# Performance work log

Hardware: AMD Instinct MI355X
Metric: run time of the kernel (lower is better)

Reference implementation:

```python
import jax, jax.numpy as jnp
import numpy as np
from jax import lax

NF, CF, LAT = 128, 3, 512          # n_filter, sobel c_factor (id+gx+gy), lat_size
NL, NC = 3, 4                      # n_layers (img 64 -> 3), n_calls
B, IMG, CH = 16, 64, 3
FIN, FH, FOUT = NF * CF, NF, 2 * NF  # dyna/res block in, hidden, out (gated -> 2*NF)
SPLIT = [NF, NF, NF, 1]
NOUT = sum(SPLIT)                  # 385
CS = NF + NF * 16 + NF * 16 + 16 * 16  # 4480 multi-cut state size
SEG = [FIN * FH, FH, FH * FH, FH, FH * FOUT, FOUT, FIN * FOUT, FOUT]
OFF = np.concatenate([[0], np.cumsum(SEG)]).astype(int)
K = int(OFF[-1])                   # hypernet output size (197376)

SOBEL_X = jnp.array([[-1., 0., 1.], [-2., 0., 2.], [-1., 0., 1.]], jnp.float32) / 8.0
SOBEL_Y = SOBEL_X.T
_g = np.exp(-0.5 * (np.arange(3) - 1.0) ** 2); _g /= _g.sum()
GAUSS = jnp.asarray(np.outer(_g, _g), jnp.float32)  # 3x3 gaussian, sigma=1


def dwconv(x, k2d):
    # depthwise conv, same 3x3 kernel for every channel, padding 1
    C = x.shape[1]
    k = jnp.broadcast_to(k2d.astype(x.dtype), (C, 1, 3, 3))
    return lax.conv_general_dilated(x, k, (1, 1), ((1, 1), (1, 1)),
                                    dimension_numbers=('NCHW', 'OIHW', 'NCHW'),
                                    feature_group_count=C)


def instnorm(x, eps=1e-5):
    m = x.mean((2, 3), keepdims=True)
    v = x.var((2, 3), keepdims=True)
    return (x - m) * lax.rsqrt(v + eps)


def conv1x1(x, w, b):  # w: [O, C]
    return jnp.einsum('bchw,oc->bohw', x, w) + b[None, :, None, None]


def lrb(x, w1, b1, w2, b2, wsc, bsc):  # LinearResidualBlock
    return x @ wsc.T + bsc + jax.nn.relu(x @ w1.T + b1) @ w2.T + b2


def _w(k, shape, fan_in):
    return jax.random.normal(k, shape, jnp.float32) / np.sqrt(fan_in)


def setup_inputs():
    ks = jax.random.split(jax.random.key(0), 24)
    z = lambda *s: jnp.zeros(s, jnp.float32)
    d = {}
    d['x'] = jax.random.normal(ks[0], (B, CH, IMG, IMG), jnp.float32)
    d['inj_lat'] = jax.random.normal(ks[1], (B, LAT), jnp.float32)
    d['leak_factor'] = jnp.float32(0.1)
    d['in_w'] = _w(ks[2], (NF, CH), CH); d['in_b'] = z(NF)
    d['fc_w1'] = _w(ks[3], (FH, FIN), FIN); d['fc_b1'] = z(FH)
    d['fc_w2'] = _w(ks[4], (FOUT, FH), FH); d['fc_b2'] = z(FOUT)
    d['fc_wsc'] = _w(ks[5], (FOUT, FIN), FIN); d['fc_bsc'] = z(FOUT)
    d['hyp_w'] = _w(ks[6], (K, LAT), LAT) * 0.1; d['hyp_b'] = z(K)
    d['lat_w'] = _w(ks[7], (NL * NC, LAT, LAT), LAT); d['lat_b'] = z(NL * NC, LAT)
    d['seed'] = _w(ks[8], (1, NF, 16, 16), NF)
    d['out_w'] = _w(ks[9], (NOUT, NF), NF); d['out_b'] = z(NOUT)
    d['l1_w1'] = _w(ks[10], (2 * LAT, CS), CS); d['l1_b1'] = z(2 * LAT)
    d['l1_w2'] = _w(ks[11], (LAT, 2 * LAT), 2 * LAT); d['l1_b2'] = z(LAT)
    d['l1_wsc'] = _w(ks[12], (LAT, CS), CS); d['l1_bsc'] = z(LAT)
    d['l2_w1'] = _w(ks[13], (LAT, LAT), LAT); d['l2_b1'] = z(LAT)
    d['l2_w2'] = _w(ks[14], (LAT, LAT), LAT); d['l2_b2'] = z(LAT)
    d['l2_wsc'] = _w(ks[15], (LAT, LAT), LAT); d['l2_bsc'] = z(LAT)
    d['fin_w'] = _w(ks[16], (LAT, LAT), LAT); d['fin_b'] = z(LAT)
    return d


def _forward(x, inj_lat, leak_factor, in_w, in_b, fc_w1, fc_b1, fc_w2, fc_b2,
             fc_wsc, fc_bsc, hyp_w, hyp_b, lat_w, lat_b, seed, out_w, out_b,
             l1_w1, l1_b1, l1_w2, l1_b2, l1_wsc, l1_bsc,
             l2_w1, l2_b1, l2_w2, l2_b2, l2_wsc, l2_bsc, fin_w, fin_b):
    out = conv1x1(x, in_w, in_b)
    leak = jnp.clip(leak_factor, 0.001, 1000.0)
    for c in range(NL * NC):
        # perception: identity + x/y sobel (c_factor=3), then instance norm
        p = jnp.concatenate([out, dwconv(out, SOBEL_X), dwconv(out, SOBEL_Y)], 1)
        p = instnorm(p)
        # static ResidualBlock (shared params)
        f = conv1x1(p, fc_wsc, fc_bsc) + conv1x1(jax.nn.relu(conv1x1(p, fc_w1, fc_b1)), fc_w2, fc_b2)
        # per-call latent expansion + hypernetwork -> per-sample 1x1 conv weights
        latc = inj_lat @ lat_w[c].T + lat_b[c]
        hk = latc @ hyp_w.T + hyp_b  # [B, K]
        w_in = hk[:, OFF[0]:OFF[1]].reshape(-1, FH, FIN); b_in = hk[:, OFF[1]:OFF[2]]
        w_md = hk[:, OFF[2]:OFF[3]].reshape(-1, FH, FH);  b_md = hk[:, OFF[3]:OFF[4]]
        w_ot = hk[:, OFF[4]:OFF[5]].reshape(-1, FOUT, FH); b_ot = hk[:, OFF[5]:OFF[6]]
        w_sc = hk[:, OFF[6]:OFF[7]].reshape(-1, FOUT, FIN); b_sc = hk[:, OFF[7]:OFF[8]]
        h = jax.nn.relu(jnp.einsum('bchw,boc->bohw', p, w_in) + b_in[:, :, None, None])
        h = jax.nn.relu(jnp.einsum('bchw,boc->bohw', h, w_md) + b_md[:, :, None, None])
        d = (jnp.einsum('bchw,boc->bohw', p, w_sc) + b_sc[:, :, None, None]
             + jnp.einsum('bchw,boc->bohw', h, w_ot) + b_ot[:, :, None, None])
        out_new = f + d  # [B, 2*NF, H, W]
        a, g = out_new[:, :NF], out_new[:, NF:]
        out = out + leak * (a * jax.nn.sigmoid(g))
        if c < NL * NC - 1 and c % NC == NC - 1:
            s = dwconv(out, GAUSS)
            # bilinear 0.5 downscale (align_corners=False) == 2x2 average
            Bn, C, H, W = s.shape
            out = s.reshape(Bn, C, H // 2, 2, W // 2, 2).mean((3, 5))
    out = out + seed  # broadcast seed [1, NF, 16, 16]
    o = conv1x1(out, out_w, out_b)  # [B, 385, 16, 16]
    f_, fh_, fw_, hw_ = o[:, :NF], o[:, NF:2 * NF], o[:, 2 * NF:3 * NF], o[:, 3 * NF:]
    bs = o.shape[0]
    cs = jnp.concatenate([f_.mean((2, 3)), fh_.mean(3).reshape(bs, -1),
                          fw_.mean(2).reshape(bs, -1), hw_.reshape(bs, -1)], 1)  # [B, 4480]
    hcs = lrb(cs, l1_w1, l1_b1, l1_w2, l1_b2, l1_wsc, l1_bsc)
    hcs = lrb(hcs, l2_w1, l2_b1, l2_w2, l2_b2, l2_wsc, l2_bsc)
    return hcs @ fin_w.T + fin_b  # [B, LAT]


def reference(x, inj_lat, leak_factor, in_w, in_b, fc_w1, fc_b1, fc_w2, fc_b2,
              fc_wsc, fc_bsc, hyp_w, hyp_b, lat_w, lat_b, seed, out_w, out_b,
              l1_w1, l1_b1, l1_w2, l1_b2, l1_wsc, l1_bsc,
              l2_w1, l2_b1, l2_w2, l2_b2, l2_wsc, l2_bsc, fin_w, fin_b):
    return _forward(x, inj_lat, leak_factor, in_w, in_b, fc_w1, fc_b1, fc_w2, fc_b2,
                    fc_wsc, fc_bsc, hyp_w, hyp_b, lat_w, lat_b, seed, out_w, out_b,
                    l1_w1, l1_b1, l1_w2, l1_b2, l1_wsc, l1_bsc,
                    l2_w1, l2_b1, l2_w2, l2_b2, l2_wsc, l2_bsc, fin_w, fin_b)
```

## Files before the change

kernel.cpp:

```cpp
#include <hip/hip_runtime.h>
#include <hip/hip_bf16.h>

typedef __hip_bfloat16 bf16;
typedef __attribute__((ext_vector_type(8))) short bf8_t;
typedef __attribute__((ext_vector_type(4))) float f4_t;

#define KHK 197376
#define OFF_WIN 0
#define OFF_BIN 49152
#define OFF_WMD 49280
#define OFF_BMD 65664
#define OFF_WOT 65792
#define OFF_BOT 98560
#define OFF_WSC 98816
#define OFF_BSC 197120

__device__ __forceinline__ float ldf(const float* p, size_t i){ return p[i]; }
__device__ __forceinline__ float ldf(const bf16* p, size_t i){ return __bfloat162float(p[i]); }
__device__ __forceinline__ void stf(float* p, size_t i, float v){ p[i] = v; }
__device__ __forceinline__ void stf(bf16* p, size_t i, float v){ p[i] = __float2bfloat16(v); }
__device__ __forceinline__ float b2f(short u){ return __uint_as_float(((unsigned)(unsigned short)u) << 16); }

typedef const __attribute__((address_space(1))) unsigned int* gas_t;
typedef __attribute__((address_space(3))) unsigned int* las_t;
__device__ __forceinline__ void gld_lds16(const void* g, void* l){
  __builtin_amdgcn_global_load_lds((gas_t)g, (las_t)l, 16, 0, 0);
}

struct Seg { const bf16* p; int klen; int ld; };

__global__ __launch_bounds__(256) void k_cvt_bf16(const float* __restrict__ in,
    bf16* __restrict__ out, size_t n){
  size_t stride = (size_t)gridDim.x * 256;
  for (size_t i = blockIdx.x*256ULL + threadIdx.x; i*8 < n; i += stride){
    float4 a = *reinterpret_cast<const float4*>(in + i*8);
    float4 c = *reinterpret_cast<const float4*>(in + i*8 + 4);
    union { bf8_t v; bf16 e[8]; } o;
    o.e[0]=__float2bfloat16(a.x); o.e[1]=__float2bfloat16(a.y);
    o.e[2]=__float2bfloat16(a.z); o.e[3]=__float2bfloat16(a.w);
    o.e[4]=__float2bfloat16(c.x); o.e[5]=__float2bfloat16(c.y);
    o.e[6]=__float2bfloat16(c.z); o.e[7]=__float2bfloat16(c.w);
    *reinterpret_cast<bf8_t*>(out + i*8) = o.v;
  }
}

__global__ __launch_bounds__(256) void k_in_conv(const float* __restrict__ x,
    const float* __restrict__ w, const float* __restrict__ b, float* __restrict__ out){
  int idx = blockIdx.x*256 + threadIdx.x;
  int c = idx & 127;
  int s = (idx >> 7) & 4095;
  int bi = idx >> 19;
  const float* xb = x + (size_t)bi*3*4096;
  out[idx] = b[c] + w[c*3]*xb[s] + w[c*3+1]*xb[4096+s] + w[c*3+2]*xb[8192+s];
}

__global__ __launch_bounds__(256) void k_sobel4(const float* __restrict__ src,
    bf16* __restrict__ p, int H, int S){
  int idx = blockIdx.x*256 + threadIdx.x;
  int c4 = (idx & 31) * 4;
  int s = (idx >> 5) % S;
  int b = idx / (S*32);
  int y = s / H, x = s - y*H;
  const float* sb = src + (size_t)b*S*128 + c4;
  float4 n[3][3];
  #pragma unroll
  for (int dy=0; dy<3; dy++)
    #pragma unroll
    for (int dx=0; dx<3; dx++){
      int yy = y + dy - 1, xx = x + dx - 1;
      if (yy>=0 && yy<H && xx>=0 && xx<H)
        n[dy][dx] = *reinterpret_cast<const float4*>(sb + (size_t)(yy*H+xx)*128);
      else
        n[dy][dx] = (float4){0.f,0.f,0.f,0.f};
    }
  float v0[4], sx[4], sy[4];
  #pragma unroll
  for (int q = 0; q < 4; q++){
    float e00=((const float*)&n[0][0])[q], e01=((const float*)&n[0][1])[q], e02=((const float*)&n[0][2])[q];
    float e10=((const float*)&n[1][0])[q], e11=((const float*)&n[1][1])[q], e12=((const float*)&n[1][2])[q];
    float e20=((const float*)&n[2][0])[q], e21=((const float*)&n[2][1])[q], e22=((const float*)&n[2][2])[q];
    v0[q] = e11;
    sx[q] = (-e00 + e02 - 2.f*e10 + 2.f*e12 - e20 + e22) * 0.125f;
    sy[q] = (-e00 - 2.f*e01 - e02 + e20 + 2.f*e21 + e22) * 0.125f;
  }
  bf16* pb = p + ((size_t)b*S + s)*384;
  union { unsigned long long u; bf16 e[4]; } o0, o1, o2;
  #pragma unroll
  for (int q = 0; q < 4; q++){
    o0.e[q] = __float2bfloat16(v0[q]);
    o1.e[q] = __float2bfloat16(sx[q]);
    o2.e[q] = __float2bfloat16(sy[q]);
  }
  *reinterpret_cast<unsigned long long*>(pb + c4)       = o0.u;
  *reinterpret_cast<unsigned long long*>(pb + 128 + c4) = o1.u;
  *reinterpret_cast<unsigned long long*>(pb + 256 + c4) = o2.u;
}

__global__ __launch_bounds__(256) void k_stats(const bf16* __restrict__ P_,
    float* __restrict__ SUMS, int S){
  __shared__ float sS[384], sQ[384];
  int b = blockIdx.y;
  int chunk = S >> 4;
  int s0 = blockIdx.x * chunk;
  int t = threadIdx.x;
  for (int i = t; i < 384; i += 256){ sS[i] = 0.f; sQ[i] = 0.f; }
  __syncthreads();
  if (t < 240){
    int oct = t % 48, ls = t / 48;
    int c8 = oct*8;
    float as[8] = {}, qs[8] = {};
    for (int s = s0 + ls; s < s0 + chunk; s += 5){
      bf8_t v = *reinterpret_cast<const bf8_t*>(P_ + ((size_t)b*S + s)*384 + c8);
      #pragma unroll
      for (int i=0;i<8;i++){ float f = b2f(v[i]); as[i]+=f; qs[i]+=f*f; }
    }
    #pragma unroll
    for (int i=0;i<8;i++){ atomicAdd(&sS[c8+i], as[i]); atomicAdd(&sQ[c8+i], qs[i]); }
  }
  __syncthreads();
  for (int i = t; i < 384; i += 256){
    atomicAdd(&SUMS[((size_t)b*384+i)*2],   sS[i]);
    atomicAdd(&SUMS[((size_t)b*384+i)*2+1], sQ[i]);
  }
}

__global__ __launch_bounds__(256) void k_hyper_all(const float* __restrict__ hw,
    const float* __restrict__ hb, const bf16* __restrict__ latb,
    bf16* __restrict__ hk_all){
  __shared__ float Sw[128][17];
  int h0 = blockIdx.x * 128;
  int tid = threadIdx.x, wid = tid >> 6, lane = tid & 63;
  int lr = lane & 15, lg = lane >> 4;
  f4_t acc[2][12];
  #pragma unroll
  for (int f=0; f<2; f++)
    #pragma unroll
    for (int j=0; j<12; j++) acc[f][j] = (f4_t){0.f,0.f,0.f,0.f};
  for (int k0 = 0; k0 < 512; k0 += 32){
    bf8_t af[2];
    #pragma unroll
    for (int f = 0; f < 2; f++){
      int h = h0 + wid*32 + f*16 + lr;
      const float* src = hw + (size_t)h*512 + k0 + lg*8;
      float4 x0 = *reinterpret_cast<const float4*>(src);
      float4 x1 = *reinterpret_cast<const float4*>(src + 4);
      union { bf8_t v; bf16 e[8]; } o;
      o.e[0]=__float2bfloat16(x0.x); o.e[1]=__float2bfloat16(x0.y);
      o.e[2]=__float2bfloat16(x0.z); o.e[3]=__float2bfloat16(x0.w);
      o.e[4]=__float2bfloat16(x1.x); o.e[5]=__float2bfloat16(x1.y);
      o.e[6]=__float2bfloat16(x1.z); o.e[7]=__float2bfloat16(x1.w);
      af[f] = o.v;
    }
    #pragma unroll
    for (int j = 0; j < 12; j++){
      bf8_t bv = *reinterpret_cast<const bf8_t*>(latb + (size_t)(j*16 + lr)*512 + k0 + lg*8);
      acc[0][j] = __builtin_amdgcn_mfma_f32_16x16x32_bf16(af[0], bv, acc[0][j], 0, 0, 0);
      acc[1][j] = __builtin_amdgcn_mfma_f32_16x16x32_bf16(af[1], bv, acc[1][j], 0, 0, 0);
    }
  }
  for (int j = 0; j < 12; j++){
    __syncthreads();
    #pragma unroll
    for (int f = 0; f < 2; f++)
      #pragma unroll
      for (int r = 0; r < 4; r++)
        Sw[wid*32 + f*16 + lg*4 + r][lr] = acc[f][j][r];
    __syncthreads();
    int bb = tid >> 4, h8 = (tid & 15) * 8;
    union { bf8_t v; bf16 e[8]; } o;
    #pragma unroll
    for (int i = 0; i < 8; i++)
      o.e[i] = __float2bfloat16(hb[h0 + h8 + i] + Sw[h8 + i][bb]);
    *reinterpret_cast<bf8_t*>(hk_all + ((size_t)j*16 + bb)*KHK + h0 + h8) = o.v;
  }
}

__global__ __launch_bounds__(256) void k_latall(const float* __restrict__ inj,
    const float* __restrict__ lat_w, const float* __restrict__ lat_b,
    bf16* __restrict__ LATB){
  int gwave = (int)((blockIdx.x*256 + threadIdx.x) >> 6);
  int lane = threadIdx.x & 63;
  int c = gwave >> 9, o = gwave & 511;
  const float* wr = lat_w + (size_t)c*262144 + (size_t)o*512;
  float acc[16] = {};
  for (int k = lane; k < 512; k += 64){
    float wv = wr[k];
    #pragma unroll
    for (int b = 0; b < 16; b++) acc[b] += wv * inj[b*512 + k];
  }
  #pragma unroll
  for (int b = 0; b < 16; b++)
    for (int off = 32; off > 0; off >>= 1) acc[b] += __shfl_down(acc[b], off);
  if (lane == 0){
    float bv = lat_b[c*512 + o];
    #pragma unroll
    for (int b = 0; b < 16; b++)
      LATB[(size_t)c*8192 + b*512 + o] = __float2bfloat16(acc[b] + bv);
  }
}

__global__ __launch_bounds__(256) void k_xform(
    const float* __restrict__ fc_w1, const float* __restrict__ fc_b1,
    const float* __restrict__ fc_w2, const float* __restrict__ fc_b2,
    const float* __restrict__ fc_wsc, const float* __restrict__ fc_bsc,
    const bf16* __restrict__ HK_, const float* __restrict__ SUMS, float Sf,
    bf16* __restrict__ Wstack, float* __restrict__ bstack,
    bf16* __restrict__ Wbig, float* __restrict__ bbig,
    bf16* __restrict__ Wmd, float* __restrict__ bmd){
  int gw = (blockIdx.x*256 + threadIdx.x) >> 6;
  int lane = threadIdx.x & 63;
  float invSf = 1.f / Sf;
  if (gw < 4096){
    int b = gw >> 8, o = gw & 255;
    const float* su = SUMS + (size_t)b*768;
    const bf16* hkb = HK_ + (size_t)b*KHK;
    float b0 = (o < 128) ? fc_b1[o] : ldf(hkb, OFF_BIN + (o-128));
    float accv = 0.f;
    bf16* dst = Wstack + ((size_t)b*256 + o)*384;
    for (int k = lane; k < 384; k += 64){
      float m = su[k*2] * invSf;
      float iv = rsqrtf(fmaxf(su[k*2+1]*invSf - m*m, 0.f) + 1e-5f);
      float wv = (o < 128) ? fc_w1[(size_t)o*384 + k]
                           : ldf(hkb, OFF_WIN + (size_t)(o-128)*384 + k);
      float w = wv * iv;
      accv += w * m;
      dst[k] = __float2bfloat16(w);
    }
    for (int off=32; off>0; off>>=1) accv += __shfl_down(accv, off);
    if (lane==0) bstack[b*256+o] = b0 - accv;
  } else if (gw < 8192){
    int r = gw - 4096; int b = r >> 8, o = r & 255;
    const float* su = SUMS + (size_t)b*768;
    const bf16* hkb = HK_ + (size_t)b*KHK;
    int cc = o & 127;
    int nr = ((cc >> 4) << 5) + ((o >> 7) << 4) + (cc & 15);
    bf16* dst = Wbig + ((size_t)b*256 + nr)*640;
    float accv = 0.f;
    for (int k = lane; k < 384; k += 64){
      float m = su[k*2] * invSf;
      float iv = rsqrtf(fmaxf(su[k*2+1]*invSf - m*m, 0.f) + 1e-5f);
      float w = (fc_wsc[(size_t)o*384 + k] + ldf(hkb, OFF_WSC + (size_t)o*384 + k)) * iv;
      accv += w * m;
      dst[k] = __float2bfloat16(w);
    }
    for (int k = lane; k < 128; k += 64){
      dst[384+k] = __float2bfloat16(fc_w2[(size_t)o*128 + k]);
      dst[512+k] = hkb[OFF_WOT + (size_t)o*128 + k];
    }
    for (int off=32; off>0; off>>=1) accv += __shfl_down(accv, off);
    if (lane==0) bbig[b*256+nr] = fc_bsc[o] + ldf(hkb, OFF_BSC+o) + fc_b2[o]
                                  + ldf(hkb, OFF_BOT+o) - accv;
  } else {
    int r = gw - 8192; int b = r >> 7, o = r & 127;
    const bf16* hkb = HK_ + (size_t)b*KHK;
    bf16* dst = Wmd + ((size_t)b*128 + o)*128;
    for (int k = lane; k < 128; k += 64)
      dst[k] = hkb[OFF_WMD + (size_t)o*128 + k];
    if (lane==0) bmd[b*128+o] = ldf(hkb, OFF_BMD + o);
  }
}

template<int RELU, int NSEG, int FUSE, class TOUT>
__global__ __launch_bounds__(256) void k_mfgemm(
    Seg s1, Seg s2, Seg s3,
    const bf16* __restrict__ W, long long wbstride, int Ktot,
    const float* __restrict__ bias, int bbstride,
    TOUT* __restrict__ OUTp, int ldc, int Mout, int S,
    const float* __restrict__ leakp){
  __shared__ short As[128][32];
  __shared__ short Bs[128][32];
  int b  = blockIdx.z;
  int s0 = blockIdx.x * 128;
  int n0 = blockIdx.y * 128;
  int tid = threadIdx.x;
  int wid = tid >> 6, lane = tid & 63;
  int wrow = (wid >> 1) * 64;
  int wcol = (wid & 1) * 64;
  int lr = lane & 15, lg = lane >> 4;
  int r0 = wid*32 + (lane >> 2);
  int c8 = (lane & 3) * 8;
  const bf16* Wb = W + (size_t)b * wbstride;
  f4_t acc[4][4] = {{}};
  int kbase = 0;
  #pragma unroll
  for (int si = 0; si < NSEG; si++){
    Seg sg = (si == 0) ? s1 : (si == 1) ? s2 : s3;
    const bf16* INb = sg.p + (size_t)b * S * sg.ld;
    const bf16* gA0 = INb + (size_t)(s0 + r0) * sg.ld + c8;
    const bf16* gA1 = INb + (size_t)(s0 + r0 + 16) * sg.ld + c8;
    const bf16* gB0 = Wb + (size_t)(n0 + r0) * Ktot + kbase + c8;
    const bf16* gB1 = Wb + (size_t)(n0 + r0 + 16) * Ktot + kbase + c8;
    for (int k0 = 0; k0 < sg.klen; k0 += 32){
      gld_lds16(gA0 + k0, &As[wid*32][0]);
      gld_lds16(gA1 + k0, &As[wid*32 + 16][0]);
      gld_lds16(gB0 + k0, &Bs[wid*32][0]);
      gld_lds16(gB1 + k0, &Bs[wid*32 + 16][0]);
      __syncthreads();
      bf8_t af[4], bfv[4];
      #pragma unroll
      for (int i = 0; i < 4; i++) af[i]  = *(const bf8_t*)(&As[wrow + i*16 + lr][lg*8]);
      #pragma unroll
      for (int j = 0; j < 4; j++) bfv[j] = *(const bf8_t*)(&Bs[wcol + j*16 + lr][lg*8]);
      #pragma unroll
      for (int i = 0; i < 4; i++)
        #pragma unroll
        for (int j = 0; j < 4; j++)
          acc[i][j] = __builtin_amdgcn_mfma_f32_16x16x32_bf16(af[i], bfv[j], acc[i][j], 0, 0, 0);
      __syncthreads();
    }
    kbase += sg.klen;
  }
  if (FUSE){
    float leak = fminf(fmaxf(leakp[0], 0.001f), 1000.f);
    float* OUTf = (float*)OUTp;
    #pragma unroll
    for (int jp = 0; jp < 2; jp++){
      int na = n0 + wcol + jp*32 + lr;
      float bva = bias[(size_t)b * bbstride + na];
      float bvg = bias[(size_t)b * bbstride + na + 16];
      int chan = ((n0 + wcol) >> 1) + jp*16 + lr;
      #pragma unroll
      for (int i = 0; i < 4; i++){
        int sr = s0 + wrow + i*16 + lg*4;
        #pragma unroll
        for (int r = 0; r < 4; r++){
          float av = acc[i][jp*2][r]   + bva;
          float gv = acc[i][jp*2+1][r] + bvg;
          size_t oidx = ((size_t)b * S + sr + r) * 128 + chan;
          OUTf[oidx] += leak * av * (1.f / (1.f + expf(-gv)));
        }
      }
    }
  } else {
    #pragma unroll
    for (int j = 0; j < 4; j++){
      int n = n0 + wcol + j*16 + lr;
      if (n >= Mout) continue;
      float bv = bias[(size_t)b * bbstride + n];
      #pragma unroll
      for (int i = 0; i < 4; i++){
        int sr = s0 + wrow + i*16 + lg*4;
        size_t base = ((size_t)b * S + sr) * ldc + n;
        #pragma unroll
        for (int r = 0; r < 4; r++){
          float v = acc[i][j][r] + bv;
          if (RELU) v = fmaxf(v, 0.f);
          stf(OUTp, base + (size_t)r * ldc, v);
        }
      }
    }
  }
}

__global__ __launch_bounds__(256) void k_blurpool(const float* __restrict__ src,
    float* __restrict__ dst, int H2, int S2){
  const float g[3] = {0.27406862f, 0.45186276f, 0.27406862f};
  int idx = blockIdx.x*256 + threadIdx.x;
  int c = idx & 127;
  int s2 = (idx >> 7) % S2;
  int b = idx / (S2*128);
  int y2 = s2 / H2, x2 = s2 - y2*H2;
  int H = H2*2;
  const float* sb = src + (size_t)b*(H*H)*128 + c;
  float acc = 0.f;
  #pragma unroll
  for (int dy2 = 0; dy2 < 2; dy2++)
    #pragma unroll
    for (int dx2 = 0; dx2 < 2; dx2++){
      int y = 2*y2 + dy2, x = 2*x2 + dx2;
      float bl = 0.f;
      #pragma unroll
      for (int i = 0; i < 3; i++)
        #pragma unroll
        for (int j = 0; j < 3; j++){
          int yy = y + i - 1, xx = x + j - 1;
          float v = (yy>=0 && yy<H && xx>=0 && xx<H) ? sb[(size_t)(yy*H+xx)*128] : 0.f;
          bl += v * g[i] * g[j];
        }
      acc += bl;
    }
  dst[idx] = acc * 0.25f;
}

__global__ __launch_bounds__(256) void k_seed(float* __restrict__ out,
    const float* __restrict__ seed){
  int idx = blockIdx.x*256 + threadIdx.x;
  int c = idx & 127;
  int s = (idx >> 7) & 255;
  out[idx] += seed[c*256 + s];
}

__global__ __launch_bounds__(256) void k_build_cs(const float* __restrict__ O,
    float* __restrict__ cs){
  int b = blockIdx.x;
  const float* Ob = O + (size_t)b*256*385;
  for (int id = threadIdx.x; id < 4480; id += 256){
    float v;
    if (id < 128){
      float s = 0; for (int t = 0; t < 256; t++) s += Ob[(size_t)t*385 + id];
      v = s * (1.f/256.f);
    } else if (id < 2176){
      int r = id - 128; int c = r >> 4, h = r & 15;
      float s = 0; for (int w = 0; w < 16; w++) s += Ob[(size_t)(h*16+w)*385 + 128 + c];
      v = s * (1.f/16.f);
    } else if (id < 4224){
      int r = id - 2176; int c = r >> 4, w = r & 15;
      float s = 0; for (int h = 0; h < 16; h++) s += Ob[(size_t)(h*16+w)*385 + 256 + c];
      v = s * (1.f/16.f);
    } else {
      v = Ob[(size_t)(id - 4224)*385 + 384];
    }
    cs[b*4480 + id] = v;
  }
}

template<int RELU, int ACCUM, class TOUT>
__global__ __launch_bounds__(256) void k_rowgemm(const float* __restrict__ IN,
    const float* __restrict__ W,
    const float* __restrict__ bias,
    TOUT* __restrict__ OUT, int M, int K){
  int wave = (int)((blockIdx.x*256 + threadIdx.x) >> 6);
  int lane = threadIdx.x & 63;
  if (wave >= M) return;
  const float* wr = W + (size_t)wave*K;
  float acc[16] = {};
  for (int k = lane; k < K; k += 64){
    float wv = wr[k];
    #pragma unroll
    for (int b = 0; b < 16; b++) acc[b] += wv * IN[b*K + k];
  }
  #pragma unroll
  for (int b = 0; b < 16; b++)
    for (int off = 32; off > 0; off >>= 1) acc[b] += __shfl_down(acc[b], off);
  if (lane == 0){
    float bv = bias[wave];
    #pragma unroll
    for (int b = 0; b < 16; b++){
      float v = acc[b] + bv;
      if (RELU) v = fmaxf(v, 0.f);
      size_t oi = (size_t)b*M + wave;
      if (ACCUM) v += ldf(OUT, oi);
      stf(OUT, oi, v);
    }
  }
}

template<int RELU1>
__global__ __launch_bounds__(256) void k_rowgemm2(const float* __restrict__ IN,
    const float* __restrict__ W1, const float* __restrict__ b1, float* __restrict__ O1, int M1,
    const float* __restrict__ W2, const float* __restrict__ b2, float* __restrict__ O2, int M2,
    int K){
  int wave = (int)((blockIdx.x*256 + threadIdx.x) >> 6);
  int lane = threadIdx.x & 63;
  if (wave >= M1 + M2) return;
  int second = (wave >= M1);
  int o = second ? (wave - M1) : wave;
  const float* wr = (second ? W2 : W1) + (size_t)o*K;
  float acc[16] = {};
  for (int k = lane; k < K; k += 64){
    float wv = wr[k];
    #pragma unroll
    for (int b = 0; b < 16; b++) acc[b] += wv * IN[b*K + k];
  }
  #pragma unroll
  for (int b = 0; b < 16; b++)
    for (int off = 32; off > 0; off >>= 1) acc[b] += __shfl_down(acc[b], off);
  if (lane == 0){
    float bv = second ? b2[o] : b1[o];
    float* OUT = second ? O2 : O1;
    int M = second ? M2 : M1;
    #pragma unroll
    for (int b = 0; b < 16; b++){
      float v = acc[b] + bv;
      if (RELU1 && !second) v = fmaxf(v, 0.f);
      OUT[(size_t)b*M + o] = v;
    }
  }
}

extern "C" void kernel_launch(void* const* d_in, const int* in_sizes, int n_in,
                              void* d_out, int out_size, void* d_ws, size_t ws_size,
                              hipStream_t stream){
  (void)in_sizes; (void)n_in; (void)out_size; (void)ws_size;
  const float* x      = (const float*)d_in[0];
  const float* inj    = (const float*)d_in[1];
  const float* leakp  = (const float*)d_in[2];
  const float* in_w   = (const float*)d_in[3];
  const float* in_b   = (const float*)d_in[4];
  const float* fc_w1  = (const float*)d_in[5];
  const float* fc_b1  = (const float*)d_in[6];
  const float* fc_w2  = (const float*)d_in[7];
  const float* fc_b2  = (const float*)d_in[8];
  const float* fc_wsc = (const float*)d_in[9];
  const float* fc_bsc = (const float*)d_in[10];
  const float* hyp_w  = (const float*)d_in[11];
  const float* hyp_b  = (const float*)d_in[12];
  const float* lat_w  = (const float*)d_in[13];
  const float* lat_b  = (const float*)d_in[14];
  const float* seed   = (const float*)d_in[15];
  const float* out_w  = (const float*)d_in[16];
  const float* out_b  = (const float*)d_in[17];
  const float* l1_w1  = (const float*)d_in[18];
  const float* l1_b1  = (const float*)d_in[19];
  const float* l1_w2  = (const float*)d_in[20];
  const float* l1_b2  = (const float*)d_in[21];
  const float* l1_wsc = (const float*)d_in[22];
  const float* l1_bsc = (const float*)d_in[23];
  const float* l2_w1  = (const float*)d_in[24];
  const float* l2_b1  = (const float*)d_in[25];
  const float* l2_w2  = (const float*)d_in[26];
  const float* l2_b2  = (const float*)d_in[27];
  const float* l2_wsc = (const float*)d_in[28];
  const float* l2_bsc = (const float*)d_in[29];
  const float* fin_w  = (const float*)d_in[30];
  const float* fin_b  = (const float*)d_in[31];

  char* ws = (char*)d_ws;
  float* OUT    = (float*)(ws);
  bf16*  P      = (bf16*)(ws + 33554432UL);
  bf16*  HG     = (bf16*)(ws + 83886080UL);
  bf16*  G2     = (bf16*)(ws + 117440512UL);
  bf16*  HKALL  = (bf16*)(ws + 134217728UL);
  bf16*  WSTK   = (bf16*)(ws + 285802496UL);
  bf16*  WBIG   = (bf16*)(ws + 288948224UL);
  bf16*  WMD    = (bf16*)(ws + 294191104UL);
  float* BSTK   = (float*)(ws + 294715392UL);
  float* BBIG   = (float*)(ws + 294731776UL);
  float* BMD    = (float*)(ws + 294748160UL);
  bf16*  LATB   = (bf16*)(ws + 294805504UL);
  bf16*  OUTB   = (bf16*)(ws + 295002112UL);
  float* OHEAD  = (float*)(ws + 296050688UL);
  bf16*  OWB    = (bf16*)(ws + 302358528UL);
  float* CS     = (float*)(ws + 302457088UL);
  float* T1     = (float*)(ws + 302743808UL);
  float* HCS    = (float*)(ws + 302809344UL);
  float* HCS2   = (float*)(ws + 302842112UL);
  float* SUMS12 = (float*)(ws + 302874880UL);
  float* OUT2   = (float*)(ws + 310378496UL);

  k_cvt_bf16<<<32, 256, 0, stream>>>(out_w, OWB, 49280ULL);
  k_in_conv<<<32768, 256, 0, stream>>>(x, in_w, in_b, OUT);

  k_latall<<<1536, 256, 0, stream>>>(inj, lat_w, lat_b, LATB);
  k_hyper_all<<<1542, 256, 0, stream>>>(hyp_w, hyp_b, LATB, HKALL);
  hipMemsetAsync(SUMS12, 0, 12*16*384*2*sizeof(float), stream);

  float* cur = OUT;
  float* alt = OUT2;
  int H = 64;
  for (int c = 0; c < 12; c++){
    int S = H*H;
    float* SUMS = SUMS12 + (size_t)c*16*768;
    k_sobel4<<<(16*S*32)/256, 256, 0, stream>>>(cur, P, H, S);
    k_stats<<<dim3(16,16), 256, 0, stream>>>(P, SUMS, S);
    k_xform<<<2560, 256, 0, stream>>>(fc_w1, fc_b1, fc_w2, fc_b2, fc_wsc, fc_bsc,
                                      HKALL + (size_t)c*16*KHK, SUMS, (float)S,
                                      WSTK, BSTK, WBIG, BBIG, WMD, BMD);
    Seg segP  = {P, 384, 384};
    Seg segH1 = {HG, 128, 256};
    Seg segHm = {HG + 128, 128, 256};
    Seg segG2 = {G2, 128, 128};
    k_mfgemm<1,1,0,bf16><<<dim3(S/128, 2, 16), 256, 0, stream>>>(
        segP, segP, segP, WSTK, 98304LL, 384, BSTK, 256, HG, 256, 256, S, nullptr);
    k_mfgemm<1,1,0,bf16><<<dim3(S/128, 1, 16), 256, 0, stream>>>(
        segHm, segHm, segHm, WMD, 16384LL, 128, BMD, 128, G2, 128, 128, S, nullptr);
    k_mfgemm<0,3,1,float><<<dim3(S/128, 2, 16), 256, 0, stream>>>(
        segP, segH1, segG2, WBIG, 163840LL, 640, BBIG, 256, cur, 128, 256, S, leakp);
    if (c == 3 || c == 7){
      int H2 = H/2, S2 = S/4;
      k_blurpool<<<(16*S2*128)/256, 256, 0, stream>>>(cur, alt, H2, S2);
      float* t = cur; cur = alt; alt = t;
      H = H2;
    }
  }

  k_seed<<<2048, 256, 0, stream>>>(cur, seed);
  k_cvt_bf16<<<256, 256, 0, stream>>>(cur, OUTB, 524288ULL);
  Seg segO = {OUTB, 128, 128};
  k_mfgemm<0,1,0,float><<<dim3(2, 4, 16), 256, 0, stream>>>(
      segO, segO, segO, OWB, 0LL, 128, out_b, 0, OHEAD, 385, 385, 256, nullptr);
  k_build_cs<<<16, 256, 0, stream>>>(OHEAD, CS);

  k_rowgemm2<1><<<384, 256, 0, stream>>>(CS, l1_w1, l1_b1, T1, 1024,
                                         l1_wsc, l1_bsc, HCS, 512, 4480);
  k_rowgemm<0,1,float><<<128, 256, 0, stream>>>(T1, l1_w2, l1_b2, HCS, 512, 1024);
  k_rowgemm2<1><<<256, 256, 0, stream>>>(HCS, l2_w1, l2_b1, T1, 512,
                                         l2_wsc, l2_bsc, HCS2, 512, 512);
  k_rowgemm<0,1,float><<<128, 256, 0, stream>>>(T1, l2_w2, l2_b2, HCS2, 512, 512);
  k_rowgemm<0,0,float><<<128, 256, 0, stream>>>(HCS2, fin_w, fin_b, (float*)d_out, 512, 512);
}
```

Before: 1.553 ms.

## Fuse middle GEMM into final gated GEMM via LDS-resident G2 tile

The hidden-layer GEMM (HG[:,128:] x Wmd) is now computed inside the final gated GEMM kernel, and its ReLU output G2 stays in shared memory instead of going through global memory. This removes one kernel launch per call and the global write and read of G2. The cost is that the middle GEMM is recomputed by both n-blocks (blockIdx.y = 0 and 1), and the extra ~34KB of LDS may lower occupancy. The seed add and bf16 conversion are also merged into one kernel.

```diff
diff --git a/kernel.cpp b/kernel.cpp
--- a/kernel.cpp
+++ b/kernel.cpp
@@ -260,13 +260,12 @@
   }
 }
 
-template<int RELU, int NSEG, int FUSE, class TOUT>
+template<int RELU, int NSEG, class TOUT>
 __global__ __launch_bounds__(256) void k_mfgemm(
     Seg s1, Seg s2, Seg s3,
     const bf16* __restrict__ W, long long wbstride, int Ktot,
     const float* __restrict__ bias, int bbstride,
-    TOUT* __restrict__ OUTp, int ldc, int Mout, int S,
-    const float* __restrict__ leakp){
+    TOUT* __restrict__ OUTp, int ldc, int Mout, int S){
   __shared__ short As[128][32];
   __shared__ short Bs[128][32];
   int b  = blockIdx.z;
@@ -310,43 +309,173 @@
     }
     kbase += sg.klen;
   }
-  if (FUSE){
-    float leak = fminf(fmaxf(leakp[0], 0.001f), 1000.f);
-    float* OUTf = (float*)OUTp;
-    #pragma unroll
-    for (int jp = 0; jp < 2; jp++){
-      int na = n0 + wcol + jp*32 + lr;
-      float bva = bias[(size_t)b * bbstride + na];
-      float bvg = bias[(size_t)b * bbstride + na + 16];
-      int chan = ((n0 + wcol) >> 1) + jp*16 + lr;
+  #pragma unroll
+  for (int j = 0; j < 4; j++){
+    int n = n0 + wcol + j*16 + lr;
+    if (n >= Mout) continue;
+    float bv = bias[(size_t)b * bbstride + n];
+    #pragma unroll
+    for (int i = 0; i < 4; i++){
+      int sr = s0 + wrow + i*16 + lg*4;
+      size_t base = ((size_t)b * S + sr) * ldc + n;
+      #pragma unroll
+      for (int r = 0; r < 4; r++){
+        float v = acc[i][j][r] + bv;
+        if (RELU) v = fmaxf(v, 0.f);
+        stf(OUTp, base + (size_t)r * ldc, v);
+      }
+    }
+  }
+}
+
+__global__ __launch_bounds__(256) void k_mfgemm23(
+    const bf16* __restrict__ P_, const bf16* __restrict__ HG_,
+    const bf16* __restrict__ Wmd, const float* __restrict__ bmd,
+    const bf16* __restrict__ Wbig, const float* __restrict__ bbig,
+    float* __restrict__ OUTf, int S, const float* __restrict__ leakp){
+  __shared__ short As[128][32];
+  __shared__ short Bs[128][32];
+  __shared__ short G2t[128][136];
+  int b  = blockIdx.z;
+  int s0 = blockIdx.x * 128;
+  int n0 = blockIdx.y * 128;
+  int tid = threadIdx.x;
+  int wid = tid >> 6, lane = tid & 63;
+  int wrow = (wid >> 1) * 64;
+  int wcol = (wid & 1) * 64;
+  int lr = lane & 15, lg = lane >> 4;
+  int r0 = wid*32 + (lane >> 2);
+  int c8 = (lane & 3) * 8;
+  bf16* G2b = (bf16*)&G2t[0][0];
+  f4_t acc[4][4] = {{}};
+  {
+    const bf16* gA0 = HG_ + ((size_t)b*S + s0 + r0) * 256 + 128 + c8;
+    const bf16* gA1 = gA0 + (size_t)16 * 256;
+    const bf16* gB0 = Wmd + (size_t)b*16384 + (size_t)r0 * 128 + c8;
+    const bf16* gB1 = gB0 + 16*128;
+    for (int k0 = 0; k0 < 128; k0 += 32){
+      gld_lds16(gA0 + k0, &As[wid*32][0]);
+      gld_lds16(gA1 + k0, &As[wid*32 + 16][0]);
+      gld_lds16(gB0 + k0, &Bs[wid*32][0]);
+      gld_lds16(gB1 + k0, &Bs[wid*32 + 16][0]);
+      __syncthreads();
+      bf8_t af[4], bfv[4];
+      #pragma unroll
+      for (int i = 0; i < 4; i++) af[i]  = *(const bf8_t*)(&As[wrow + i*16 + lr][lg*8]);
+      #pragma unroll
+      for (int j = 0; j < 4; j++) bfv[j] = *(const bf8_t*)(&Bs[wcol + j*16 + lr][lg*8]);
+      #pragma unroll
+      for (int i = 0; i < 4; i++)
+        #pragma unroll
+        for (int j = 0; j < 4; j++)
+          acc[i][j] = __builtin_amdgcn_mfma_f32_16x16x32_bf16(af[i], bfv[j], acc[i][j], 0, 0, 0);
+      __syncthreads();
+    }
+    const float* bmdb = bmd + b*128;
+    #pragma unroll
+    for (int j = 0; j < 4; j++){
+      int col = wcol + j*16 + lr;
+      float bv = bmdb[col];
       #pragma unroll
       for (int i = 0; i < 4; i++){
-        int sr = s0 + wrow + i*16 + lg*4;
+        int row = wrow + i*16 + lg*4;
         #pragma unroll
-        for (int r = 0; r < 4; r++){
-          float av = acc[i][jp*2][r]   + bva;
-          float gv = acc[i][jp*2+1][r] + bvg;
-          size_t oidx = ((size_t)b * S + sr + r) * 128 + chan;
-          OUTf[oidx] += leak * av * (1.f / (1.f + expf(-gv)));
-        }
+        for (int r = 0; r < 4; r++)
+          stf(G2b, (size_t)(row + r)*136 + col, fmaxf(acc[i][j][r] + bv, 0.f));
       }
     }
-  } else {
-    #pragma unroll
-    for (int j = 0; j < 4; j++){
-      int n = n0 + wcol + j*16 + lr;
-      if (n >= Mout) continue;
-      float bv = bias[(size_t)b * bbstride + n];
-      #pragma unroll
-      for (int i = 0; i < 4; i++){
-        int sr = s0 + wrow + i*16 + lg*4;
-        size_t base = ((size_t)b * S + sr) * ldc + n;
+    #pragma unroll
+    for (int i = 0; i < 4; i++)
+      #pragma unroll
+      for (int j = 0; j < 4; j++)
+        acc[i][j] = (f4_t){0.f,0.f,0.f,0.f};
+    __syncthreads();
+  }
+  const bf16* Wb = Wbig + (size_t)b * 163840;
+  {
+    const bf16* gA0 = P_ + ((size_t)b*S + s0 + r0) * 384 + c8;
+    const bf16* gA1 = gA0 + (size_t)16 * 384;
+    const bf16* gB0 = Wb + (size_t)(n0 + r0) * 640 + c8;
+    const bf16* gB1 = gB0 + (size_t)16*640;
+    for (int k0 = 0; k0 < 384; k0 += 32){
+      gld_lds16(gA0 + k0, &As[wid*32][0]);
+      gld_lds16(gA1 + k0, &As[wid*32 + 16][0]);
+      gld_lds16(gB0 + k0, &Bs[wid*32][0]);
+      gld_lds16(gB1 + k0, &Bs[wid*32 + 16][0]);
+      __syncthreads();
+      bf8_t af[4], bfv[4];
+      #pragma unroll
+      for (int i = 0; i < 4; i++) af[i]  = *(const bf8_t*)(&As[wrow + i*16 + lr][lg*8]);
+      #pragma unroll
+      for (int j = 0; j < 4; j++) bfv[j] = *(const bf8_t*)(&Bs[wcol + j*16 + lr][lg*8]);
+      #pragma unroll
+      for (int i = 0; i < 4; i++)
         #pragma unroll
-        for (int r = 0; r < 4; r++){
-          float v = acc[i][j][r] + bv;
-          if (RELU) v = fmaxf(v, 0.f);
-          stf(OUTp, base + (size_t)r * ldc, v);
-        }
+        for (int j = 0; j < 4; j++)
+          acc[i][j] = __builtin_amdgcn_mfma_f32_16x16x32_bf16(af[i], bfv[j], acc[i][j], 0, 0, 0);
+      __syncthreads();
+    }
+  }
+  {
+    const bf16* gA0 = HG_ + ((size_t)b*S + s0 + r0) * 256 + c8;
+    const bf16* gA1 = gA0 + (size_t)16 * 256;
+    const bf16* gB0 = Wb + (size_t)(n0 + r0) * 640 + 384 + c8;
+    const bf16* gB1 = gB0 + (size_t)16*640;
+    for (int k0 = 0; k0 < 128; k0 += 32){
+      gld_lds16(gA0 + k0, &As[wid*32][0]);
+      gld_lds16(gA1 + k0, &As[wid*32 + 16][0]);
+      gld_lds16(gB0 + k0, &Bs[wid*32][0]);
+      gld_lds16(gB1 + k0, &Bs[wid*32 + 16][0]);
+      __syncthreads();
+      bf8_t af[4], bfv[4];
+      #pragma unroll
+      for (int i = 0; i < 4; i++) af[i]  = *(const bf8_t*)(&As[wrow + i*16 + lr][lg*8]);
+      #pragma unroll
+      for (int j = 0; j < 4; j++) bfv[j] = *(const bf8_t*)(&Bs[wcol + j*16 + lr][lg*8]);
+      #pragma unroll
+      for (int i = 0; i < 4; i++)
+        #pragma unroll
+        for (int j = 0; j < 4; j++)
+          acc[i][j] = __builtin_amdgcn_mfma_f32_16x16x32_bf16(af[i], bfv[j], acc[i][j], 0, 0, 0);
+      __syncthreads();
+    }
+  }
+  {
+    const bf16* gB0 = Wb + (size_t)(n0 + r0) * 640 + 512 + c8;
+    const bf16* gB1 = gB0 + (size_t)16*640;
+    for (int k0 = 0; k0 < 128; k0 += 32){
+      gld_lds16(gB0 + k0, &Bs[wid*32][0]);
+      gld_lds16(gB1 + k0, &Bs[wid*32 + 16][0]);
+      __syncthreads();
+      bf8_t af[4], bfv[4];
+      #pragma unroll
+      for (int i = 0; i < 4; i++) af[i]  = *(const bf8_t*)(&G2t[wrow + i*16 + lr][k0 + lg*8]);
+      #pragma unroll
+      for (int j = 0; j < 4; j++) bfv[j] = *(const bf8_t*)(&Bs[wcol + j*16 + lr][lg*8]);
+      #pragma unroll
+      for (int i = 0; i < 4; i++)
+        #pragma unroll
+        for (int j = 0; j < 4; j++)
+          acc[i][j] = __builtin_amdgcn_mfma_f32_16x16x32_bf16(af[i], bfv[j], acc[i][j], 0, 0, 0);
+      __syncthreads();
+    }
+  }
+  float leak = fminf(fmaxf(leakp[0], 0.001f), 1000.f);
+  #pragma unroll
+  for (int jp = 0; jp < 2; jp++){
+    int na = n0 + wcol + jp*32 + lr;
+    float bva = bbig[(size_t)b * 256 + na];
+    float bvg = bbig[(size_t)b * 256 + na + 16];
+    int chan = ((n0 + wcol) >> 1) + jp*16 + lr;
+    #pragma unroll
+    for (int i = 0; i < 4; i++){
+      int sr = s0 + wrow + i*16 + lg*4;
+      #pragma unroll
+      for (int r = 0; r < 4; r++){
+        float av = acc[i][jp*2][r]   + bva;
+        float gv = acc[i][jp*2+1][r] + bvg;
+        size_t oidx = ((size_t)b * S + sr + r) * 128 + chan;
+        OUTf[oidx] += leak * av * (1.f / (1.f + expf(-gv)));
       }
     }
   }
@@ -382,12 +511,12 @@
   dst[idx] = acc * 0.25f;
 }
 
-__global__ __launch_bounds__(256) void k_seed(float* __restrict__ out,
-    const float* __restrict__ seed){
+__global__ __launch_bounds__(256) void k_seedcvt(const float* __restrict__ in,
+    const float* __restrict__ seed, bf16* __restrict__ out){
   int idx = blockIdx.x*256 + threadIdx.x;
   int c = idx & 127;
   int s = (idx >> 7) & 255;
-  out[idx] += seed[c*256 + s];
+  out[idx] = __float2bfloat16(in[idx] + seed[c*256 + s]);
 }
 
 __global__ __launch_bounds__(256) void k_build_cs(const float* __restrict__ O,
@@ -519,7 +648,6 @@
   float* OUT    = (float*)(ws);
   bf16*  P      = (bf16*)(ws + 33554432UL);
   bf16*  HG     = (bf16*)(ws + 83886080UL);
-  bf16*  G2     = (bf16*)(ws + 117440512UL);
   bf16*  HKALL  = (bf16*)(ws + 134217728UL);
   bf16*  WSTK   = (bf16*)(ws + 285802496UL);
   bf16*  WBIG   = (bf16*)(ws + 288948224UL);
@@ -543,7 +671,7 @@
 
   k_latall<<<1536, 256, 0, stream>>>(inj, lat_w, lat_b, LATB);
   k_hyper_all<<<1542, 256, 0, stream>>>(hyp_w, hyp_b, LATB, HKALL);
-  hipMemsetAsync(SUMS12, 0, 12*16*384*2*sizeof(float), stream);
+  (void)hipMemsetAsync(SUMS12, 0, 12*16*384*2*sizeof(float), stream);
 
   float* cur = OUT;
   float* alt = OUT2;
@@ -557,15 +685,10 @@
                                       HKALL + (size_t)c*16*KHK, SUMS, (float)S,
                                       WSTK, BSTK, WBIG, BBIG, WMD, BMD);
     Seg segP  = {P, 384, 384};
-    Seg segH1 = {HG, 128, 256};
-    Seg segHm = {HG + 128, 128, 256};
-    Seg segG2 = {G2, 128, 128};
-    k_mfgemm<1,1,0,bf16><<<dim3(S/128, 2, 16), 256, 0, stream>>>(
-        segP, segP, segP, WSTK, 98304LL, 384, BSTK, 256, HG, 256, 256, S, nullptr);
-    k_mfgemm<1,1,0,bf16><<<dim3(S/128, 1, 16), 256, 0, stream>>>(
-        segHm, segHm, segHm, WMD, 16384LL, 128, BMD, 128, G2, 128, 128, S, nullptr);
-    k_mfgemm<0,3,1,float><<<dim3(S/128, 2, 16), 256, 0, stream>>>(
-        segP, segH1, segG2, WBIG, 163840LL, 640, BBIG, 256, cur, 128, 256, S, leakp);
+    k_mfgemm<1,1,bf16><<<dim3(S/128, 2, 16), 256, 0, stream>>>(
+        segP, segP, segP, WSTK, 98304LL, 384, BSTK, 256, HG, 256, 256, S);
+    k_mfgemm23<<<dim3(S/128, 2, 16), 256, 0, stream>>>(
+        P, HG, WMD, BMD, WBIG, BBIG, cur, S, leakp);
     if (c == 3 || c == 7){
       int H2 = H/2, S2 = S/4;
       k_blurpool<<<(16*S2*128)/256, 256, 0, stream>>>(cur, alt, H2, S2);
@@ -574,11 +697,10 @@
     }
   }
 
-  k_seed<<<2048, 256, 0, stream>>>(cur, seed);
-  k_cvt_bf16<<<256, 256, 0, stream>>>(cur, OUTB, 524288ULL);
+  k_seedcvt<<<2048, 256, 0, stream>>>(cur, seed, OUTB);
   Seg segO = {OUTB, 128, 128};
-  k_mfgemm<0,1,0,float><<<dim3(2, 4, 16), 256, 0, stream>>>(
-      segO, segO, segO, OWB, 0LL, 128, out_b, 0, OHEAD, 385, 385, 256, nullptr);
+  k_mfgemm<0,1,float><<<dim3(2, 4, 16), 256, 0, stream>>>(
+      segO, segO, segO, OWB, 0LL, 128, out_b, 0, OHEAD, 385, 385, 256);
   k_build_cs<<<16, 256, 0, stream>>>(OHEAD, CS);
 
   k_rowgemm2<1><<<384, 256, 0, stream>>>(CS, l1_w1, l1_b1, T1, 1024,
```

Result: faster. 1.482 ms (-4.6%).
